# Kernel tuning notes

Measured on AMD Instinct MI355X. Metric: run time of the kernel, lower is better.

Reference implementation:

```python
import jax, jax.numpy as jnp
import numpy as np

DIM = 1024
HEADS = 8
HEAD_DIM = DIM // HEADS
FFN = 4096
B, N = 32, 1024
EPS = 1e-5


def layer_norm(x, g, b):
    mu = jnp.mean(x, axis=-1, keepdims=True)
    var = jnp.mean(jnp.square(x - mu), axis=-1, keepdims=True)
    return (x - mu) * jax.lax.rsqrt(var + EPS) * g + b


def setup_inputs() -> dict:
    key = jax.random.key(0)
    ks = jax.random.split(key, 10)
    s = 0.02
    return {
        "x": jax.random.normal(ks[0], (B, N, DIM), dtype=jnp.float32),
        "haltingscore": jnp.zeros((B, N), dtype=jnp.float32),
        "Wq": jax.random.normal(ks[1], (DIM, DIM), dtype=jnp.float32) * s,
        "Wkv": jax.random.normal(ks[2], (DIM, 2 * DIM), dtype=jnp.float32) * s,
        "Wp": jax.random.normal(ks[3], (DIM, DIM), dtype=jnp.float32) * s,
        "bp": jnp.zeros((DIM,), dtype=jnp.float32),
        "W1": jax.random.normal(ks[4], (DIM, FFN), dtype=jnp.float32) * s,
        "b1": jnp.zeros((FFN,), dtype=jnp.float32),
        "W2": jax.random.normal(ks[5], (FFN, DIM), dtype=jnp.float32) * s,
        "b2": jnp.zeros((DIM,), dtype=jnp.float32),
        "ln1_g": jnp.ones((DIM,), dtype=jnp.float32),
        "ln1_b": jnp.zeros((DIM,), dtype=jnp.float32),
        "ln2_g": jnp.ones((DIM,), dtype=jnp.float32),
        "ln2_b": jnp.zeros((DIM,), dtype=jnp.float32),
    }


def reference(x, haltingscore, Wq, Wkv, Wp, bp, W1, b1, W2, b2,
              ln1_g, ln1_b, ln2_g, ln2_b):
    b, n, c = x.shape
    scale = HEAD_DIM ** -0.5
    # ---- EfficientAttention (explicit QK^T softmax V) ----
    q = (x @ Wq).reshape(b, n, HEADS, HEAD_DIM).transpose(0, 2, 1, 3)  # bhnd
    kv = (x @ Wkv).reshape(b, n, 2, HEADS, HEAD_DIM).transpose(2, 0, 3, 1, 4)
    k, v = kv[0], kv[1]                                               # bhnd
    attn = jax.nn.softmax(jnp.einsum('bhnd,bhmd->bhnm', q, k) * scale, axis=-1)
    o = jnp.einsum('bhnm,bhmd->bhnd', attn, v)
    o = o.transpose(0, 2, 1, 3).reshape(b, n, c)
    o = o @ Wp + bp
    attn_mean = jnp.mean(attn, axis=1)                                # (B, N, N)
    # ---- residual + LN1 ----
    h = layer_norm(x + o, ln1_g, ln1_b)
    # ---- FFN + residual + LN2 ----
    ff = jax.nn.relu(h @ W1 + b1) @ W2 + b2
    out = layer_norm(h + ff, ln2_g, ln2_b)
    # ---- halting score update ----
    a = jax.nn.softmax(jnp.sum(attn_mean, axis=1), axis=-1)           # (B, N)
    halting = haltingscore + a
    return (out, halting, a)
```

## Files before the change

### kernel.cpp

```cpp
#include <hip/hip_runtime.h>
#include <hip/hip_bf16.h>
#include <stdint.h>

#define DIMC 1024
#define HEADS 8
#define HDIM 128
#define FFND 4096
#define BATCH 32
#define SEQ 1024
#define SROWS (BATCH*SEQ)
#define QSTR 3072

typedef unsigned short u16;
typedef short short4v __attribute__((ext_vector_type(4)));
typedef short short8 __attribute__((ext_vector_type(8)));
typedef float f32x4 __attribute__((ext_vector_type(4)));
typedef __bf16 bf16x8 __attribute__((ext_vector_type(8)));

__device__ __forceinline__ u16 f2bf(float f) {
    union { float f; uint32_t u; } x{f};
    uint32_t r = x.u + 0x7FFFu + ((x.u >> 16) & 1u);
    return (u16)(r >> 16);
}
__device__ __forceinline__ float bf2f(u16 h) {
    union { uint32_t u; float f; } x;
    x.u = ((uint32_t)h) << 16;
    return x.f;
}

__device__ __forceinline__ f32x4 mfma16(short8 a, short8 b, f32x4 c) {
    return __builtin_amdgcn_mfma_f32_16x16x32_bf16(
        __builtin_bit_cast(bf16x8, a), __builtin_bit_cast(bf16x8, b), c, 0, 0, 0);
}

__device__ __forceinline__ void gload_lds16(const u16* g, u16* lds) {
    __builtin_amdgcn_global_load_lds(
        (const __attribute__((address_space(1))) uint32_t*)g,
        (__attribute__((address_space(3))) uint32_t*)lds, 16, 0, 0);
}

#define DPP_RORADD(x, ctrl) do {                                               \
    int _t = __builtin_amdgcn_mov_dpp(__builtin_bit_cast(int, (x)), (ctrl),    \
                                      0xf, 0xf, true);                         \
    (x) += __builtin_bit_cast(float, _t); } while (0)

__device__ __forceinline__ short8 p2frag(f32x4 p0, f32x4 p1, int lane) {
    uint32_t a, b, c, d;
    asm("v_cvt_pk_bf16_f32 %0, %1, %2" : "=v"(a) : "v"(p0[0]), "v"(p0[1]));
    asm("v_cvt_pk_bf16_f32 %0, %1, %2" : "=v"(b) : "v"(p0[2]), "v"(p0[3]));
    asm("v_cvt_pk_bf16_f32 %0, %1, %2" : "=v"(c) : "v"(p1[0]), "v"(p1[1]));
    asm("v_cvt_pk_bf16_f32 %0, %1, %2" : "=v"(d) : "v"(p1[2]), "v"(p1[3]));
    uint32_t ax = (uint32_t)__shfl_xor((int)a, 32);
    uint32_t bx = (uint32_t)__shfl_xor((int)b, 32);
    uint32_t cx = (uint32_t)__shfl_xor((int)c, 32);
    uint32_t dx = (uint32_t)__shfl_xor((int)d, 32);
    const bool up = (lane & 32) != 0;
    uint32_t P = up ? cx : a, Q = up ? c : ax;
    uint32_t R = up ? dx : b, S = up ? d : bx;
    uint32_t Px = (uint32_t)__shfl_xor((int)P, 16);
    uint32_t Qx = (uint32_t)__shfl_xor((int)Q, 16);
    uint32_t Rx = (uint32_t)__shfl_xor((int)R, 16);
    uint32_t Sx = (uint32_t)__shfl_xor((int)S, 16);
    const bool odd = (lane & 16) != 0;
    uint32_t w0 = odd ? Qx : P,  w1 = odd ? Sx : R;
    uint32_t w2 = odd ? Q  : Px, w3 = odd ? S  : Rx;
    union { uint32_t w[4]; short8 s; } u;
    u.w[0] = w0; u.w[1] = w1; u.w[2] = w2; u.w[3] = w3;
    return u.s;
}

__global__ __launch_bounds__(256) void k_cast(const float* __restrict__ in,
                                              u16* __restrict__ out, int n4) {
    int i = blockIdx.x * 256 + threadIdx.x;
    if (i < n4) {
        f32x4 v = ((const f32x4*)in)[i];
        uint32_t lo = f2bf(v[0]) | ((uint32_t)f2bf(v[1]) << 16);
        uint32_t hi = f2bf(v[2]) | ((uint32_t)f2bf(v[3]) << 16);
        ((uint2*)out)[i] = make_uint2(lo, hi);
    }
}

__global__ __launch_bounds__(256) void k_transpose_cast(const float* __restrict__ W,
                                                        u16* __restrict__ Wt,
                                                        int K, int N) {
    __shared__ u16 tile[32][33];
    int n0 = blockIdx.x * 32, k0 = blockIdx.y * 32;
    int tx = threadIdx.x, ty = threadIdx.y;
#pragma unroll
    for (int i = 0; i < 32; i += 8)
        tile[ty + i][tx] = f2bf(W[(size_t)(k0 + ty + i) * N + n0 + tx]);
    __syncthreads();
#pragma unroll
    for (int i = 0; i < 32; i += 8)
        Wt[(size_t)(n0 + ty + i) * K + k0 + tx] = tile[tx][ty + i];
}

template<bool OUT_BF16, bool RELU, bool BIAS, bool VSPLIT>
__global__ __launch_bounds__(512, 2) void k_gemm256(const u16* __restrict__ A,
                                                    const u16* __restrict__ Bt,
                                                    const float* __restrict__ bias,
                                                    void* __restrict__ C,
                                                    u16* __restrict__ Vt,
                                                    int M, int N, int K) {
    union Smem {
        struct { u16 A[4][8192]; u16 B[4][8192]; } k;
        u16 ob[64 * 264];
        float of[64 * 268];
        u16 vt[256 * 66];
    };
    __shared__ Smem smem;
    const int tid = threadIdx.x;
    const int lane = tid & 63, wv = tid >> 6;
    const int wm = wv >> 2, wn = wv & 3;
    const int l15 = lane & 15, lg = lane >> 4;
    const int gx = gridDim.x;
    const int nwg = gx * gridDim.y;
    const int id = blockIdx.y * gx + blockIdx.x;
    const int id2 = (id & 7) * (nwg >> 3) + (id >> 3);
    const int row0 = (id2 / gx) << 8, col0 = (id2 % gx) << 8;
    const int NT = K >> 5;

#define STAGE_A(tt) {                                                          \
    int _t = (tt);                                                             \
    _Pragma("unroll")                                                          \
    for (int i = 0; i < 2; ++i) {                                              \
        int blk = wv * 2 + i;                                                  \
        gload_lds16(A + (size_t)(row0 + blk * 16 + l15) * K + _t * 32 + lg * 8,\
                    &smem.k.A[_t & 3][blk * 512]);                             \
    } }
#define STAGE_B(tt) {                                                          \
    int _t = (tt);                                                             \
    _Pragma("unroll")                                                          \
    for (int i = 0; i < 2; ++i) {                                              \
        int blk = wv * 2 + i;                                                  \
        gload_lds16(Bt + (size_t)(col0 + blk * 16 + l15) * K + _t * 32 + lg * 8,\
                    &smem.k.B[_t & 3][blk * 512]);                             \
    } }

    STAGE_A(0); STAGE_B(0);
    STAGE_A(1); STAGE_B(1);
    STAGE_A(2); STAGE_B(2);

    f32x4 acc[8][4] = {};
    for (int t = 0; t < NT; ++t) {
        const int slot = t & 3;
        if (t <= NT - 3)      asm volatile("s_waitcnt vmcnt(8)" ::: "memory");
        else if (t == NT - 2) asm volatile("s_waitcnt vmcnt(4)" ::: "memory");
        else                  asm volatile("s_waitcnt vmcnt(0)" ::: "memory");
        __builtin_amdgcn_s_barrier();
        __builtin_amdgcn_sched_barrier(0);

        const u16* Ab = &smem.k.A[slot][(wm * 8) * 512];
        const u16* Bb = &smem.k.B[slot][(wn * 4) * 512];

        if (t + 3 < NT) STAGE_A(t + 3);
        short8 bf[4], af[4];
#pragma unroll
        for (int n = 0; n < 4; ++n) bf[n] = *(const short8*)(Bb + n * 512 + lane * 8);
#pragma unroll
        for (int m = 0; m < 4; ++m) af[m] = *(const short8*)(Ab + m * 512 + lane * 8);
        __builtin_amdgcn_s_setprio(1);
#pragma unroll
        for (int m = 0; m < 4; ++m)
#pragma unroll
            for (int n = 0; n < 4; ++n)
                acc[m][n] = mfma16(af[m], bf[n], acc[m][n]);
        __builtin_amdgcn_s_setprio(0);

        if (t + 3 < NT) STAGE_B(t + 3);
#pragma unroll
        for (int m = 0; m < 4; ++m) af[m] = *(const short8*)(Ab + (4 + m) * 512 + lane * 8);
        __builtin_amdgcn_s_setprio(1);
#pragma unroll
        for (int m = 0; m < 4; ++m)
#pragma unroll
            for (int n = 0; n < 4; ++n)
                acc[4 + m][n] = mfma16(af[m], bf[n], acc[4 + m][n]);
        __builtin_amdgcn_s_setprio(0);
    }
#undef STAGE_A
#undef STAGE_B

    const bool vpath = VSPLIT && (col0 >= 2048);
    __syncthreads();
#pragma unroll
    for (int s = 0; s < 4; ++s) {
        if (s) __syncthreads();
        if (wm == (s >> 1)) {
            const int mb4 = (s & 1) * 4;
#pragma unroll
            for (int mm = 0; mm < 4; ++mm)
#pragma unroll
                for (int n = 0; n < 4; ++n) {
                    int c = wn * 64 + n * 16 + l15;
                    float bv = BIAS ? bias[col0 + c] : 0.f;
#pragma unroll
                    for (int j = 0; j < 4; ++j) {
                        int lr = mm * 16 + lg * 4 + j;
                        float v = acc[mb4 + mm][n][j] + bv;
                        if (RELU) v = fmaxf(v, 0.f);
                        if (vpath)         smem.vt[c * 66 + lr] = f2bf(v);
                        else if (OUT_BF16) smem.ob[lr * 264 + c] = f2bf(v);
                        else               smem.of[lr * 268 + c] = v;
                    }
                }
        }
        __syncthreads();
        const int gr0 = row0 + s * 64;
        if (vpath) {
            const int bb = gr0 >> 10;
            const int mb = gr0 & 1023;
#pragma unroll
            for (int it = 0; it < 4; ++it) {
                int idx = it * 512 + tid;
                int dc = idx >> 3, mseg = idx & 7;
                int hh = (col0 - 2048 + dc) >> 7;
                int dd = (col0 - 2048 + dc) & 127;
                *(short8*)(Vt + ((size_t)(bb * 8 + hh)) * (HDIM * SEQ)
                              + (size_t)dd * SEQ + mb + mseg * 8) =
                    *(const short8*)(&smem.vt[dc * 66 + mseg * 8]);
            }
        } else if (OUT_BF16) {
#pragma unroll
            for (int it = 0; it < 4; ++it) {
                int idx = it * 512 + tid;
                int r = idx >> 5, seg = idx & 31;
                *(short8*)((u16*)C + (size_t)(gr0 + r) * N + col0 + seg * 8) =
                    *(const short8*)(&smem.ob[r * 264 + seg * 8]);
            }
        } else {
#pragma unroll
            for (int it = 0; it < 8; ++it) {
                int idx = it * 512 + tid;
                int r = idx >> 6, seg = idx & 63;
                *(f32x4*)((float*)C + (size_t)(gr0 + r) * N + col0 + seg * 4) =
                    *(const f32x4*)(&smem.of[r * 268 + seg * 4]);
            }
        }
    }
}

__global__ __launch_bounds__(256, 3) void k_attn(const u16* __restrict__ QKV,
                                                 const u16* __restrict__ Vt,
                                                 u16* __restrict__ O,
                                                 float* __restrict__ csp) {
    union Sm {
        u16 K2[2][8192];
        struct { u16 Kl[2][4096]; u16 Vl[2][4096]; } pb;
    };
    __shared__ Sm sm;
    __shared__ float cs[1024];
    const int id = blockIdx.x;
    const int id2 = (id & 7) * 256 + (id >> 3);
    const int qt = id2 & 7, bh = id2 >> 3;
    const int b = bh >> 3, h = bh & 7;
    const int tid = threadIdx.x, lane = tid & 63, wv = tid >> 6;
    const int l15 = lane & 15, lg = lane >> 4;

    for (int i = tid; i < 1024; i += 256) cs[i] = 0.f;

    const int q0 = qt * 128 + wv * 32;
    const u16* qbaseA = QKV + (size_t)(b * SEQ + q0 + l15) * QSTR + h * HDIM + lg * 8;
    const u16* qbaseB = qbaseA + (size_t)16 * QSTR;
    short8 qfA[4], qfB[4];
#pragma unroll
    for (int kk = 0; kk < 4; ++kk) {
        qfA[kk] = *(const short8*)(qbaseA + kk * 32);
        qfB[kk] = *(const short8*)(qbaseB + kk * 32);
    }
    const float CEXP = 0.12751743f;
    const u16* kbase = QKV + (size_t)(b * SEQ) * QSTR + 1024 + h * HDIM;
    const u16* vtb = Vt + (size_t)bh * HDIM * SEQ;

#define STAGE_K2(tt) { _Pragma("unroll")                                        \
    for (int i = 0; i < 4; ++i) {                                               \
        gload_lds16(kbase + (size_t)((tt) * 64 + wv * 16 + l15) * QSTR          \
                    + i * 32 + lg * 8, &sm.K2[(tt) & 1][(wv * 4 + i) * 512]); } }
#define STAGE_K(tt) { _Pragma("unroll")                                         \
    for (int i = 0; i < 2; ++i) { int c = wv * 2 + i;                           \
        gload_lds16(kbase + (size_t)((tt) * 32 + (c >> 2) * 16 + l15) * QSTR    \
                    + (c & 3) * 32 + lg * 8, &sm.pb.Kl[(tt) & 1][c * 512]); } }
#define STAGE_V(tt) { _Pragma("unroll")                                         \
    for (int i = 0; i < 2; ++i) { int c = wv * 2 + i;                           \
        gload_lds16(vtb + (size_t)(c * 16 + l15) * SEQ + (tt) * 32 + lg * 8,    \
                    &sm.pb.Vl[(tt) & 1][c * 512]); } }

    STAGE_K2(0);
    asm volatile("s_waitcnt vmcnt(0)" ::: "memory");
    __builtin_amdgcn_s_barrier();
    f32x4 rsA4 = {0.f, 0.f, 0.f, 0.f}, rsB4 = {0.f, 0.f, 0.f, 0.f};
    for (int t = 0; t < 16; ++t) {
        if (t < 15) STAGE_K2(t + 1);
        const u16* Kp = &sm.K2[t & 1][0];
        __builtin_amdgcn_s_setprio(1);
#pragma unroll
        for (int j = 0; j < 4; j += 2) {
            f32x4 s0 = {0.f,0.f,0.f,0.f}, s1 = {0.f,0.f,0.f,0.f};
            f32x4 s2 = {0.f,0.f,0.f,0.f}, s3 = {0.f,0.f,0.f,0.f};
#pragma unroll
            for (int kk = 0; kk < 4; ++kk) {
                short8 k0 = *(const short8*)(Kp + (j * 4 + kk) * 512 + lane * 8);
                short8 k1 = *(const short8*)(Kp + ((j + 1) * 4 + kk) * 512 + lane * 8);
                s0 = mfma16(k0, qfA[kk], s0);
                s1 = mfma16(k0, qfB[kk], s1);
                s2 = mfma16(k1, qfA[kk], s2);
                s3 = mfma16(k1, qfB[kk], s3);
            }
#pragma unroll
            for (int r = 0; r < 4; ++r) {
                rsA4[r] += __builtin_amdgcn_exp2f(s0[r] * CEXP)
                         + __builtin_amdgcn_exp2f(s2[r] * CEXP);
                rsB4[r] += __builtin_amdgcn_exp2f(s1[r] * CEXP)
                         + __builtin_amdgcn_exp2f(s3[r] * CEXP);
            }
        }
        __builtin_amdgcn_s_setprio(0);
        asm volatile("s_waitcnt vmcnt(0)" ::: "memory");
        __builtin_amdgcn_s_barrier();
    }
    float rsA = (rsA4[0] + rsA4[1]) + (rsA4[2] + rsA4[3]);
    float rsB = (rsB4[0] + rsB4[1]) + (rsB4[2] + rsB4[3]);
    rsA += __shfl_xor(rsA, 16); rsA += __shfl_xor(rsA, 32);
    rsB += __shfl_xor(rsB, 16); rsB += __shfl_xor(rsB, 32);
    const float lgA = __builtin_amdgcn_logf(rsA);
    const float lgB = __builtin_amdgcn_logf(rsB);

    STAGE_K(0); STAGE_V(0);
    asm volatile("s_waitcnt vmcnt(0)" ::: "memory");
    __builtin_amdgcn_s_barrier();
    f32x4 odA[8] = {}, odB[8] = {};
    for (int t = 0; t < 32; ++t) {
        const int m0 = t * 32;
        if (t < 31) { STAGE_K(t + 1); STAGE_V(t + 1); }
        const u16* Kp = &sm.pb.Kl[t & 1][0];
        f32x4 sA0 = {0.f,0.f,0.f,0.f}, sA1 = {0.f,0.f,0.f,0.f};
        f32x4 sB0 = {0.f,0.f,0.f,0.f}, sB1 = {0.f,0.f,0.f,0.f};
        __builtin_amdgcn_s_setprio(1);
#pragma unroll
        for (int kk = 0; kk < 4; ++kk) {
            short8 k0 = *(const short8*)(Kp + kk * 512 + lane * 8);
            short8 k1 = *(const short8*)(Kp + (4 + kk) * 512 + lane * 8);
            sA0 = mfma16(k0, qfA[kk], sA0);
            sA1 = mfma16(k1, qfA[kk], sA1);
            sB0 = mfma16(k0, qfB[kk], sB0);
            sB1 = mfma16(k1, qfB[kk], sB1);
        }
        __builtin_amdgcn_s_setprio(0);
        f32x4 pA0, pA1, pB0, pB1;
#pragma unroll
        for (int r = 0; r < 4; ++r) {
            pA0[r] = __builtin_amdgcn_exp2f(__builtin_fmaf(sA0[r], CEXP, -lgA));
            pA1[r] = __builtin_amdgcn_exp2f(__builtin_fmaf(sA1[r], CEXP, -lgA));
            pB0[r] = __builtin_amdgcn_exp2f(__builtin_fmaf(sB0[r], CEXP, -lgB));
            pB1[r] = __builtin_amdgcn_exp2f(__builtin_fmaf(sB1[r], CEXP, -lgB));
        }
        float csv[8];
#pragma unroll
        for (int r = 0; r < 4; ++r) {
            csv[r]     = pA0[r] + pB0[r];
            csv[4 + r] = pA1[r] + pB1[r];
        }
#pragma unroll
        for (int j2 = 0; j2 < 8; ++j2) {
            DPP_RORADD(csv[j2], 0x128);
            DPP_RORADD(csv[j2], 0x124);
            DPP_RORADD(csv[j2], 0x122);
            DPP_RORADD(csv[j2], 0x121);
        }
        float cval = csv[0];
        cval = (l15 == 1) ? csv[1] : cval;
        cval = (l15 == 2) ? csv[2] : cval;
        cval = (l15 == 3) ? csv[3] : cval;
        cval = (l15 == 4) ? csv[4] : cval;
        cval = (l15 == 5) ? csv[5] : cval;
        cval = (l15 == 6) ? csv[6] : cval;
        cval = (l15 == 7) ? csv[7] : cval;
        if (l15 < 8) {
            int mw = (l15 < 4) ? (lg * 4 + l15) : (16 + lg * 4 + (l15 - 4));
            atomicAdd(&cs[m0 + mw], cval);
        }
        short8 paA = p2frag(pA0, pA1, lane);
        short8 paB = p2frag(pB0, pB1, lane);
        const u16* Vb_ = &sm.pb.Vl[t & 1][0];
        __builtin_amdgcn_s_setprio(1);
#pragma unroll
        for (int db = 0; db < 8; ++db) {
            short8 vf = *(const short8*)(Vb_ + db * 512 + lane * 8);
            odA[db] = mfma16(paA, vf, odA[db]);
            odB[db] = mfma16(paB, vf, odB[db]);
        }
        __builtin_amdgcn_s_setprio(0);
        asm volatile("s_waitcnt vmcnt(0)" ::: "memory");
        __builtin_amdgcn_s_barrier();
    }
#undef STAGE_K2
#undef STAGE_K
#undef STAGE_V
    __syncthreads();
    u16* obA = O + (size_t)(b * SEQ + q0 + lg * 4) * DIMC + h * HDIM + l15;
    u16* obB = obA + (size_t)16 * DIMC;
#pragma unroll
    for (int db = 0; db < 8; ++db)
#pragma unroll
        for (int r = 0; r < 4; ++r) {
            obA[(size_t)r * DIMC + db * 16] = f2bf(odA[db][r]);
            obB[(size_t)r * DIMC + db * 16] = f2bf(odB[db][r]);
        }
    for (int m = tid; m < 1024; m += 256)
        csp[((size_t)bh * 8 + qt) * 1024 + m] = cs[m];
}

__global__ __launch_bounds__(256) void k_ln1(const float* __restrict__ xa,
                                             const u16* __restrict__ pj,
                                             const float* __restrict__ g,
                                             const float* __restrict__ bt,
                                             u16* __restrict__ ob) {
    const int row = blockIdx.x;
    const int t = threadIdx.x, lane = t & 63, wv = t >> 6;
    f32x4 va = ((const f32x4*)(xa + (size_t)row * DIMC))[t];
    short4v hv = ((const short4v*)(pj + (size_t)row * DIMC))[t];
    f32x4 s;
#pragma unroll
    for (int j = 0; j < 4; ++j) s[j] = va[j] + bf2f((u16)hv[j]);
    float sum = s[0] + s[1] + s[2] + s[3];
    float sq = s[0]*s[0] + s[1]*s[1] + s[2]*s[2] + s[3]*s[3];
#pragma unroll
    for (int o = 1; o < 64; o <<= 1) { sum += __shfl_xor(sum, o); sq += __shfl_xor(sq, o); }
    __shared__ float red[8];
    if (lane == 0) { red[wv] = sum; red[4 + wv] = sq; }
    __syncthreads();
    sum = red[0] + red[1] + red[2] + red[3];
    sq  = red[4] + red[5] + red[6] + red[7];
    float mu = sum * (1.f / DIMC);
    float rstd = rsqrtf(sq * (1.f / DIMC) - mu * mu + 1e-5f);
    f32x4 gg = ((const f32x4*)g)[t];
    f32x4 bb = ((const f32x4*)bt)[t];
    uint32_t lo, hi;
    float o0 = (s[0] - mu) * rstd * gg[0] + bb[0];
    float o1 = (s[1] - mu) * rstd * gg[1] + bb[1];
    float o2 = (s[2] - mu) * rstd * gg[2] + bb[2];
    float o3 = (s[3] - mu) * rstd * gg[3] + bb[3];
    lo = f2bf(o0) | ((uint32_t)f2bf(o1) << 16);
    hi = f2bf(o2) | ((uint32_t)f2bf(o3) << 16);
    ((uint2*)(ob + (size_t)row * DIMC))[t] = make_uint2(lo, hi);
}

__global__ __launch_bounds__(256) void k_ln2(const u16* __restrict__ xa,
                                             const u16* __restrict__ f2,
                                             const float* __restrict__ g,
                                             const float* __restrict__ bt,
                                             float* __restrict__ of) {
    const int row = blockIdx.x;
    const int t = threadIdx.x, lane = t & 63, wv = t >> 6;
    short4v hv = ((const short4v*)(xa + (size_t)row * DIMC))[t];
    short4v fv = ((const short4v*)(f2 + (size_t)row * DIMC))[t];
    f32x4 s;
#pragma unroll
    for (int j = 0; j < 4; ++j) s[j] = bf2f((u16)hv[j]) + bf2f((u16)fv[j]);
    float sum = s[0] + s[1] + s[2] + s[3];
    float sq = s[0]*s[0] + s[1]*s[1] + s[2]*s[2] + s[3]*s[3];
#pragma unroll
    for (int o = 1; o < 64; o <<= 1) { sum += __shfl_xor(sum, o); sq += __shfl_xor(sq, o); }
    __shared__ float red[8];
    if (lane == 0) { red[wv] = sum; red[4 + wv] = sq; }
    __syncthreads();
    sum = red[0] + red[1] + red[2] + red[3];
    sq  = red[4] + red[5] + red[6] + red[7];
    float mu = sum * (1.f / DIMC);
    float rstd = rsqrtf(sq * (1.f / DIMC) - mu * mu + 1e-5f);
    f32x4 gg = ((const f32x4*)g)[t];
    f32x4 bb = ((const f32x4*)bt)[t];
    f32x4 o4;
#pragma unroll
    for (int j = 0; j < 4; ++j) o4[j] = (s[j] - mu) * rstd * gg[j] + bb[j];
    ((f32x4*)(of + (size_t)row * DIMC))[t] = o4;
}

__global__ __launch_bounds__(256) void k_halt(const float* __restrict__ csp,
                                              const float* __restrict__ hs,
                                              float* __restrict__ halt_out,
                                              float* __restrict__ a_out) {
    const int b = blockIdx.x, t = threadIdx.x, lane = t & 63, wv = t >> 6;
    const float* base = csp + (size_t)b * 65536;
    float acc[4] = {0.f, 0.f, 0.f, 0.f};
    for (int s2 = 0; s2 < 64; ++s2) {
#pragma unroll
        for (int j = 0; j < 4; ++j) acc[j] += base[(size_t)s2 * 1024 + j * 256 + t];
    }
    float mx = -1e30f;
#pragma unroll
    for (int j = 0; j < 4; ++j) { acc[j] *= 0.125f; mx = fmaxf(mx, acc[j]); }
#pragma unroll
    for (int o = 1; o < 64; o <<= 1) mx = fmaxf(mx, __shfl_xor(mx, o));
    __shared__ float red[8];
    if (lane == 0) red[wv] = mx;
    __syncthreads();
    mx = fmaxf(fmaxf(red[0], red[1]), fmaxf(red[2], red[3]));
    float e[4]; float sum = 0.f;
#pragma unroll
    for (int j = 0; j < 4; ++j) { e[j] = __expf(acc[j] - mx); sum += e[j]; }
#pragma unroll
    for (int o = 1; o < 64; o <<= 1) sum += __shfl_xor(sum, o);
    if (lane == 0) red[4 + wv] = sum;
    __syncthreads();
    sum = red[4] + red[5] + red[6] + red[7];
    float inv = 1.f / sum;
#pragma unroll
    for (int j = 0; j < 4; ++j) {
        int m = j * 256 + t;
        float a = e[j] * inv;
        a_out[b * SEQ + m] = a;
        halt_out[b * SEQ + m] = hs[b * SEQ + m] + a;
    }
}

extern "C" void kernel_launch(void* const* d_in, const int* in_sizes, int n_in,
                              void* d_out, int out_size, void* d_ws, size_t ws_size,
                              hipStream_t stream) {
    (void)in_sizes; (void)n_in; (void)out_size; (void)ws_size;
    const float* x   = (const float*)d_in[0];
    const float* hs  = (const float*)d_in[1];
    const float* Wq  = (const float*)d_in[2];
    const float* Wkv = (const float*)d_in[3];
    const float* Wp  = (const float*)d_in[4];
    const float* bp  = (const float*)d_in[5];
    const float* W1  = (const float*)d_in[6];
    const float* b1  = (const float*)d_in[7];
    const float* W2  = (const float*)d_in[8];
    const float* b2  = (const float*)d_in[9];
    const float* g1  = (const float*)d_in[10];
    const float* be1 = (const float*)d_in[11];
    const float* g2  = (const float*)d_in[12];
    const float* be2 = (const float*)d_in[13];

    float* out = (float*)d_out;
    float* halt_out = out + (size_t)SROWS * DIMC;
    float* a_out = halt_out + SROWS;

    char* w = (char*)d_ws;
    const size_t MB = 1024 * 1024;
    u16*  xb    = (u16*)(w);
    u16*  qkv   = (u16*)(w + 64 * MB);
    u16*  Vt    = (u16*)(w + 256 * MB);
    u16*  WqkvT = (u16*)(w + 320 * MB);
    u16*  WpT   = (u16*)(w + 326 * MB);
    u16*  W1T   = (u16*)(w + 328 * MB);
    u16*  W2T   = (u16*)(w + 336 * MB);
    float* csp  = (float*)(w + 344 * MB);
    u16*  o_b   = (u16*)(w);
    u16*  projb = (u16*)(w + 64 * MB);
    u16*  hb    = (u16*)(w);
    u16*  ff1   = (u16*)(w + 64 * MB);
    u16*  ff2b  = (u16*)(w + 192 * MB);

    dim3 tb(32, 8);
    k_cast<<<SROWS * DIMC / 4 / 256, 256, 0, stream>>>(x, xb, SROWS * DIMC / 4);
    k_transpose_cast<<<dim3(DIMC / 32, DIMC / 32), tb, 0, stream>>>(Wq, WqkvT, DIMC, DIMC);
    k_transpose_cast<<<dim3(2 * DIMC / 32, DIMC / 32), tb, 0, stream>>>(
        Wkv, WqkvT + (size_t)DIMC * DIMC, DIMC, 2 * DIMC);
    k_transpose_cast<<<dim3(DIMC / 32, DIMC / 32), tb, 0, stream>>>(Wp, WpT, DIMC, DIMC);
    k_transpose_cast<<<dim3(FFND / 32, DIMC / 32), tb, 0, stream>>>(W1, W1T, DIMC, FFND);
    k_transpose_cast<<<dim3(DIMC / 32, FFND / 32), tb, 0, stream>>>(W2, W2T, FFND, DIMC);
    k_gemm256<true, false, false, true><<<dim3(QSTR / 256, SROWS / 256), 512, 0, stream>>>(
        xb, WqkvT, nullptr, qkv, Vt, SROWS, QSTR, DIMC);
    k_attn<<<2048, 256, 0, stream>>>(qkv, Vt, o_b, csp);
    k_gemm256<true, false, true, false><<<dim3(DIMC / 256, SROWS / 256), 512, 0, stream>>>(
        o_b, WpT, bp, projb, nullptr, SROWS, DIMC, DIMC);
    k_ln1<<<SROWS, 256, 0, stream>>>(x, projb, g1, be1, hb);
    for (int c = 0; c < 2; ++c) {
        const size_t ro = (size_t)c * 16384;
        k_gemm256<true, true, true, false><<<dim3(FFND / 256, 16384 / 256), 512, 0, stream>>>(
            hb + ro * DIMC, W1T, b1, ff1, nullptr, 16384, FFND, DIMC);
        k_gemm256<true, false, true, false><<<dim3(DIMC / 256, 16384 / 256), 512, 0, stream>>>(
            ff1, W2T, b2, ff2b, nullptr, 16384, DIMC, FFND);
        k_ln2<<<16384, 256, 0, stream>>>(hb + ro * DIMC, ff2b, g2, be2, out + ro * DIMC);
    }
    k_halt<<<BATCH, 256, 0, stream>>>(csp, hs, halt_out, a_out);
}
```

Before: 1.442 ms.

## Use permlane swaps in P fragment shuffle and reuse buffers to cut traffic

The bf16 P-fragment repack in attention now uses the permlane32/permlane16 swap builtins when available, replacing ds_bpermute-style shuffles plus selects. The attention output is written into the unused V slot of the qkv buffer (stride QSTR), and the projection GEMM gains an lda parameter so it can read it in place. LN1 now reads the bf16 copy of x instead of the fp32 input and writes its result in place, which halves the residual read traffic. In exchange the residual in LN1 uses the bf16-rounded x rather than fp32, so precision drops slightly.

```diff
diff --git a/kernel.cpp b/kernel.cpp
--- a/kernel.cpp
+++ b/kernel.cpp
@@ -16,6 +16,7 @@
 typedef short short8 __attribute__((ext_vector_type(8)));
 typedef float f32x4 __attribute__((ext_vector_type(4)));
 typedef __bf16 bf16x8 __attribute__((ext_vector_type(8)));
+typedef unsigned uintv2 __attribute__((ext_vector_type(2)));
 
 __device__ __forceinline__ u16 f2bf(float f) {
     union { float f; uint32_t u; } x{f};
@@ -50,20 +51,42 @@
     asm("v_cvt_pk_bf16_f32 %0, %1, %2" : "=v"(b) : "v"(p0[2]), "v"(p0[3]));
     asm("v_cvt_pk_bf16_f32 %0, %1, %2" : "=v"(c) : "v"(p1[0]), "v"(p1[1]));
     asm("v_cvt_pk_bf16_f32 %0, %1, %2" : "=v"(d) : "v"(p1[2]), "v"(p1[3]));
-    uint32_t ax = (uint32_t)__shfl_xor((int)a, 32);
-    uint32_t bx = (uint32_t)__shfl_xor((int)b, 32);
-    uint32_t cx = (uint32_t)__shfl_xor((int)c, 32);
-    uint32_t dx = (uint32_t)__shfl_xor((int)d, 32);
-    const bool up = (lane & 32) != 0;
-    uint32_t P = up ? cx : a, Q = up ? c : ax;
-    uint32_t R = up ? dx : b, S = up ? d : bx;
-    uint32_t Px = (uint32_t)__shfl_xor((int)P, 16);
-    uint32_t Qx = (uint32_t)__shfl_xor((int)Q, 16);
-    uint32_t Rx = (uint32_t)__shfl_xor((int)R, 16);
-    uint32_t Sx = (uint32_t)__shfl_xor((int)S, 16);
-    const bool odd = (lane & 16) != 0;
-    uint32_t w0 = odd ? Qx : P,  w1 = odd ? Sx : R;
-    uint32_t w2 = odd ? Q  : Px, w3 = odd ? S  : Rx;
+    uint32_t P, Q, R, S;
+#if __has_builtin(__builtin_amdgcn_permlane32_swap)
+    {
+        uintv2 pq = __builtin_amdgcn_permlane32_swap(a, c, false, false);
+        uintv2 rs = __builtin_amdgcn_permlane32_swap(b, d, false, false);
+        P = pq[0]; Q = pq[1]; R = rs[0]; S = rs[1];
+    }
+#else
+    {
+        uint32_t ax = (uint32_t)__shfl_xor((int)a, 32);
+        uint32_t bx = (uint32_t)__shfl_xor((int)b, 32);
+        uint32_t cx = (uint32_t)__shfl_xor((int)c, 32);
+        uint32_t dx = (uint32_t)__shfl_xor((int)d, 32);
+        const bool up = (lane & 32) != 0;
+        P = up ? cx : a; Q = up ? c : ax;
+        R = up ? dx : b; S = up ? d : bx;
+    }
+#endif
+    uint32_t w0, w1, w2, w3;
+#if __has_builtin(__builtin_amdgcn_permlane16_swap)
+    {
+        uintv2 w02 = __builtin_amdgcn_permlane16_swap(P, Q, false, false);
+        uintv2 w13 = __builtin_amdgcn_permlane16_swap(R, S, false, false);
+        w0 = w02[0]; w2 = w02[1]; w1 = w13[0]; w3 = w13[1];
+    }
+#else
+    {
+        uint32_t Px = (uint32_t)__shfl_xor((int)P, 16);
+        uint32_t Qx = (uint32_t)__shfl_xor((int)Q, 16);
+        uint32_t Rx = (uint32_t)__shfl_xor((int)R, 16);
+        uint32_t Sx = (uint32_t)__shfl_xor((int)S, 16);
+        const bool odd = (lane & 16) != 0;
+        w0 = odd ? Qx : P;  w1 = odd ? Sx : R;
+        w2 = odd ? Q  : Px; w3 = odd ? S  : Rx;
+    }
+#endif
     union { uint32_t w[4]; short8 s; } u;
     u.w[0] = w0; u.w[1] = w1; u.w[2] = w2; u.w[3] = w3;
     return u.s;
@@ -101,7 +124,7 @@
                                                     const float* __restrict__ bias,
                                                     void* __restrict__ C,
                                                     u16* __restrict__ Vt,
-                                                    int M, int N, int K) {
+                                                    int M, int N, int K, int lda) {
     union Smem {
         struct { u16 A[4][8192]; u16 B[4][8192]; } k;
         u16 ob[64 * 264];
@@ -125,7 +148,7 @@
     _Pragma("unroll")                                                          \
     for (int i = 0; i < 2; ++i) {                                              \
         int blk = wv * 2 + i;                                                  \
-        gload_lds16(A + (size_t)(row0 + blk * 16 + l15) * K + _t * 32 + lg * 8,\
+        gload_lds16(A + (size_t)(row0 + blk * 16 + l15) * lda + _t * 32 + lg * 8,\
                     &smem.k.A[_t & 3][blk * 512]);                             \
     } }
 #define STAGE_B(tt) {                                                          \
@@ -397,31 +420,30 @@
 #undef STAGE_K
 #undef STAGE_V
     __syncthreads();
-    u16* obA = O + (size_t)(b * SEQ + q0 + lg * 4) * DIMC + h * HDIM + l15;
-    u16* obB = obA + (size_t)16 * DIMC;
+    u16* obA = O + (size_t)(b * SEQ + q0 + lg * 4) * QSTR + h * HDIM + l15;
+    u16* obB = obA + (size_t)16 * QSTR;
 #pragma unroll
     for (int db = 0; db < 8; ++db)
 #pragma unroll
         for (int r = 0; r < 4; ++r) {
-            obA[(size_t)r * DIMC + db * 16] = f2bf(odA[db][r]);
-            obB[(size_t)r * DIMC + db * 16] = f2bf(odB[db][r]);
+            obA[(size_t)r * QSTR + db * 16] = f2bf(odA[db][r]);
+            obB[(size_t)r * QSTR + db * 16] = f2bf(odB[db][r]);
         }
     for (int m = tid; m < 1024; m += 256)
         csp[((size_t)bh * 8 + qt) * 1024 + m] = cs[m];
 }
 
-__global__ __launch_bounds__(256) void k_ln1(const float* __restrict__ xa,
+__global__ __launch_bounds__(256) void k_ln1(u16* xio,
                                              const u16* __restrict__ pj,
                                              const float* __restrict__ g,
-                                             const float* __restrict__ bt,
-                                             u16* __restrict__ ob) {
+                                             const float* __restrict__ bt) {
     const int row = blockIdx.x;
     const int t = threadIdx.x, lane = t & 63, wv = t >> 6;
-    f32x4 va = ((const f32x4*)(xa + (size_t)row * DIMC))[t];
+    short4v va = ((const short4v*)(xio + (size_t)row * DIMC))[t];
     short4v hv = ((const short4v*)(pj + (size_t)row * DIMC))[t];
     f32x4 s;
 #pragma unroll
-    for (int j = 0; j < 4; ++j) s[j] = va[j] + bf2f((u16)hv[j]);
+    for (int j = 0; j < 4; ++j) s[j] = bf2f((u16)va[j]) + bf2f((u16)hv[j]);
     float sum = s[0] + s[1] + s[2] + s[3];
     float sq = s[0]*s[0] + s[1]*s[1] + s[2]*s[2] + s[3]*s[3];
 #pragma unroll
@@ -442,7 +464,7 @@
     float o3 = (s[3] - mu) * rstd * gg[3] + bb[3];
     lo = f2bf(o0) | ((uint32_t)f2bf(o1) << 16);
     hi = f2bf(o2) | ((uint32_t)f2bf(o3) << 16);
-    ((uint2*)(ob + (size_t)row * DIMC))[t] = make_uint2(lo, hi);
+    ((uint2*)(xio + (size_t)row * DIMC))[t] = make_uint2(lo, hi);
 }
 
 __global__ __launch_bounds__(256) void k_ln2(const u16* __restrict__ xa,
@@ -547,9 +569,9 @@
     u16*  W1T   = (u16*)(w + 328 * MB);
     u16*  W2T   = (u16*)(w + 336 * MB);
     float* csp  = (float*)(w + 344 * MB);
-    u16*  o_b   = (u16*)(w);
-    u16*  projb = (u16*)(w + 64 * MB);
-    u16*  hb    = (u16*)(w);
+    u16*  o_b   = qkv + 2048;
+    u16*  projb = (u16*)(w + 256 * MB);
+    u16*  hb    = xb;
     u16*  ff1   = (u16*)(w + 64 * MB);
     u16*  ff2b  = (u16*)(w + 192 * MB);
 
@@ -562,17 +584,17 @@
     k_transpose_cast<<<dim3(FFND / 32, DIMC / 32), tb, 0, stream>>>(W1, W1T, DIMC, FFND);
     k_transpose_cast<<<dim3(DIMC / 32, FFND / 32), tb, 0, stream>>>(W2, W2T, FFND, DIMC);
     k_gemm256<true, false, false, true><<<dim3(QSTR / 256, SROWS / 256), 512, 0, stream>>>(
-        xb, WqkvT, nullptr, qkv, Vt, SROWS, QSTR, DIMC);
+        xb, WqkvT, nullptr, qkv, Vt, SROWS, QSTR, DIMC, DIMC);
     k_attn<<<2048, 256, 0, stream>>>(qkv, Vt, o_b, csp);
     k_gemm256<true, false, true, false><<<dim3(DIMC / 256, SROWS / 256), 512, 0, stream>>>(
-        o_b, WpT, bp, projb, nullptr, SROWS, DIMC, DIMC);
-    k_ln1<<<SROWS, 256, 0, stream>>>(x, projb, g1, be1, hb);
+        o_b, WpT, bp, projb, nullptr, SROWS, DIMC, DIMC, QSTR);
+    k_ln1<<<SROWS, 256, 0, stream>>>(xb, projb, g1, be1);
     for (int c = 0; c < 2; ++c) {
         const size_t ro = (size_t)c * 16384;
         k_gemm256<true, true, true, false><<<dim3(FFND / 256, 16384 / 256), 512, 0, stream>>>(
-            hb + ro * DIMC, W1T, b1, ff1, nullptr, 16384, FFND, DIMC);
+            hb + ro * DIMC, W1T, b1, ff1, nullptr, 16384, FFND, DIMC, DIMC);
         k_gemm256<true, false, true, false><<<dim3(DIMC / 256, 16384 / 256), 512, 0, stream>>>(
-            ff1, W2T, b2, ff2b, nullptr, 16384, DIMC, FFND);
+            ff1, W2T, b2, ff2b, nullptr, 16384, DIMC, FFND, FFND);
         k_ln2<<<16384, 256, 0, stream>>>(hb + ro * DIMC, ff2b, g2, be2, out + ro * DIMC);
     }
     k_halt<<<BATCH, 256, 0, stream>>>(csp, hs, halt_out, a_out);
```

After: 1.433 ms, median of 3. Within noise of the previous version (-0.6%).
